# Kernel tuning notes

Hardware: AMD Instinct MI355X
Metric: run time of the kernel (lower is better)

Reference implementation:

```python
import jax, jax.numpy as jnp
import numpy as np

N, D, H = 2048, 128, 40


def setup_inputs() -> dict:
    key = jax.random.key(0)
    kx, kw, kv = jax.random.split(key, 3)
    X = jax.random.normal(kx, (N, D), dtype=jnp.float32)
    # nn.Parameter(torch.randn(D, D) / D) per head, stacked over H
    W = jax.random.normal(kw, (H, D, D), dtype=jnp.float32) / D
    V = jax.random.normal(kv, (H, D, D), dtype=jnp.float32) / D
    return {"X": X, "W": W, "V": V}


def reference(X, W, V):
    d = X.shape[1]
    # scores[h] = X @ W[h] @ X.T / sqrt(D)   -> [H, N, N]
    XW = jnp.einsum("nd,hde->hne", X, W)
    scores = jnp.einsum("hne,me->hnm", XW, X) / jnp.sqrt(jnp.asarray(d, X.dtype))
    # softmax over dim=1 of the 2D per-head score matrix == last axis here
    weights = jax.nn.softmax(scores, axis=-1) + 1e-8
    # A[h] = weights[h] @ X @ V[h]; output = sum over heads -> [N, D]
    XV = jnp.einsum("md,hde->hme", X, V)
    out = jnp.einsum("hnm,hme->ne", weights, XV)
    return out
```

## Files before the change

kernel.cpp:

```cpp
#include <hip/hip_runtime.h>
#include <hip/hip_bf16.h>
#include <stdint.h>

#define N 2048
#define D 128
#define H 40

typedef __attribute__((ext_vector_type(8))) short short8;
typedef __attribute__((ext_vector_type(4))) float float4v;
typedef __attribute__((ext_vector_type(8))) float float8v;
typedef __attribute__((ext_vector_type(16))) float float16v;
typedef __attribute__((ext_vector_type(8))) _Float16 half8v;

static __device__ __forceinline__ unsigned short f32_to_bf16(float f) {
  unsigned int u = __builtin_bit_cast(unsigned int, f);
  unsigned int rounding = 0x7FFFu + ((u >> 16) & 1u);
  return (unsigned short)((u + rounding) >> 16);
}

static __device__ __forceinline__ unsigned int pk2(float lo, float hi) {
  return (unsigned int)f32_to_bf16(lo) | ((unsigned int)f32_to_bf16(hi) << 16);
}

static __device__ __forceinline__ unsigned int pk2f(float lo, float hi) {
  unsigned int a = __builtin_bit_cast(unsigned int, lo) + 0x8000u;
  unsigned int b = __builtin_bit_cast(unsigned int, hi) + 0x8000u;
  return __builtin_amdgcn_perm(b, a, 0x07060302u);
}

static __device__ __forceinline__ unsigned long long pack4(float x0, float x1,
                                                           float x2, float x3) {
  return (unsigned long long)pk2(x0, x1) | ((unsigned long long)pk2(x2, x3) << 32);
}

static __device__ __forceinline__ float fast_exp2(float x) {
#if __has_builtin(__builtin_amdgcn_exp2f)
  return __builtin_amdgcn_exp2f(x);
#else
  return __expf(0.69314718056f * x);
#endif
}

static __device__ __forceinline__ void load_lds16(const void* g, void* l) {
  __builtin_amdgcn_global_load_lds(
      (const __attribute__((address_space(1))) unsigned int*)g,
      (__attribute__((address_space(3))) unsigned int*)l, 16, 0, 0);
}

#define MFMA32(a, b, c) __builtin_amdgcn_mfma_f32_32x32x16_bf16((a), (b), (c), 0, 0, 0)

static __device__ __forceinline__ void regs_to_bfrags(const float16v c, int hh,
                                                      short8& f0, short8& f1) {
  unsigned int a0 = pk2f(c[0], c[1]),   a1 = pk2f(c[2], c[3]);
  unsigned int a2 = pk2f(c[4], c[5]),   a3 = pk2f(c[6], c[7]);
  unsigned int a4 = pk2f(c[8], c[9]),   a5 = pk2f(c[10], c[11]);
  unsigned int a6 = pk2f(c[12], c[13]), a7 = pk2f(c[14], c[15]);
  unsigned int x0 = __shfl_xor(hh ? a0 : a2, 32);
  unsigned int x1 = __shfl_xor(hh ? a1 : a3, 32);
  unsigned int x2 = __shfl_xor(hh ? a4 : a6, 32);
  unsigned int x3 = __shfl_xor(hh ? a5 : a7, 32);
  uint4 u0 = {hh ? x0 : a0, hh ? x1 : a1, hh ? a2 : x0, hh ? a3 : x1};
  uint4 u1 = {hh ? x2 : a4, hh ? x3 : a5, hh ? a6 : x2, hh ? a7 : x3};
  f0 = __builtin_bit_cast(short8, u0);
  f1 = __builtin_bit_cast(short8, u1);
}

static __device__ __forceinline__ void regs_to_pfrags(const float16v s, int hh,
                                                      float& lsum, short8& f0,
                                                      short8& f1) {
  float e[16];
  float acc = 0.0f;
#pragma unroll
  for (int i = 0; i < 16; i++) { e[i] = fast_exp2(s[i]); acc += e[i]; }
  lsum += acc;
  unsigned int a0 = pk2f(e[0], e[1]),   a1 = pk2f(e[2], e[3]);
  unsigned int a2 = pk2f(e[4], e[5]),   a3 = pk2f(e[6], e[7]);
  unsigned int a4 = pk2f(e[8], e[9]),   a5 = pk2f(e[10], e[11]);
  unsigned int a6 = pk2f(e[12], e[13]), a7 = pk2f(e[14], e[15]);
  unsigned int x0 = __shfl_xor(hh ? a0 : a2, 32);
  unsigned int x1 = __shfl_xor(hh ? a1 : a3, 32);
  unsigned int x2 = __shfl_xor(hh ? a4 : a6, 32);
  unsigned int x3 = __shfl_xor(hh ? a5 : a7, 32);
  uint4 u0 = {hh ? x0 : a0, hh ? x1 : a1, hh ? a2 : x0, hh ? a3 : x1};
  uint4 u1 = {hh ? x2 : a4, hh ? x3 : a5, hh ? a6 : x2, hh ? a7 : x3};
  f0 = __builtin_bit_cast(short8, u0);
  f1 = __builtin_bit_cast(short8, u1);
}

static __device__ __forceinline__ void stage_64x256(const char* gbase, size_t stride,
                                                    int colOff, char* lds, int wave,
                                                    int lane) {
#pragma unroll
  for (int i = 0; i < 4; i++) {
    int r = wave * 16 + i * 4 + (lane >> 4);
    int us = (lane & 15) ^ (r & 15);
    load_lds16(gbase + (size_t)r * stride + colOff + us * 16,
               lds + (wave * 16 + i * 4) * 256);
  }
}
static __device__ __forceinline__ void stage_128x256(const char* gbase, size_t stride,
                                                     char* lds, int wave, int lane) {
#pragma unroll
  for (int i = 0; i < 8; i++) {
    int r = wave * 32 + i * 4 + (lane >> 4);
    int us = (lane & 15) ^ (r & 15);
    load_lds16(gbase + (size_t)r * stride + us * 16, lds + (wave * 32 + i * 4) * 256);
  }
}
static __device__ __forceinline__ void stage_128x128(const char* gbase, size_t stride,
                                                     int colOff, char* lds, int wave,
                                                     int lane) {
#pragma unroll
  for (int i = 0; i < 4; i++) {
    int m = wave * 16 + i * 4 + (lane >> 4);
    int u = (lane & 15) ^ (m & 15);
    int grow = 2 * m + (u >> 3);
    load_lds16(gbase + (size_t)grow * stride + colOff + (u & 7) * 16,
               lds + (wave * 16 + i * 4) * 256);
  }
}
static __device__ __forceinline__ short8 read_macro(const char* lds, int row, int kunit) {
  int m = row >> 1;
  int u = ((row & 1) << 3) | kunit;
  return *(const short8*)(lds + m * 256 + ((u ^ (m & 15)) * 16));
}

__global__ __launch_bounds__(256)
void xconv_kernel(const float* __restrict__ X, unsigned short* __restrict__ Xb,
                  unsigned short* __restrict__ XbT) {
  const int n0 = blockIdx.x * 128;
  const int tid = threadIdx.x;
  __shared__ __align__(16) unsigned short Lt[128 * 136];
  for (int i = tid; i < 128 * 32; i += 256) {
    int row = i >> 5, c4 = (i & 31) * 4;
    float4v x = *(const float4v*)(X + (size_t)(n0 + row) * D + c4);
    unsigned long long p = pack4(x.x, x.y, x.z, x.w);
    *(unsigned long long*)(Lt + row * 136 + c4) = p;
    *(unsigned long long*)(Xb + (size_t)(n0 + row) * D + c4) = p;
  }
  __syncthreads();
  for (int i = tid; i < 128 * 16; i += 256) {
    int d = i >> 4, g = i & 15;
    short8 v;
#pragma unroll
    for (int j = 0; j < 8; j++) v[j] = (short)Lt[(g * 8 + j) * 136 + d];
    *(short8*)(XbT + (size_t)d * N + n0 + g * 8) = v;
  }
}

__global__ __launch_bounds__(256)
void wvconv_kernel(const float* __restrict__ W, const float* __restrict__ V,
                   unsigned short* __restrict__ Wt, unsigned short* __restrict__ Vt) {
  const int b = blockIdx.x;
  const int mat = (b >= H) ? 1 : 0;
  const int h = mat ? b - H : b;
  const float* src = (mat ? V : W) + (size_t)h * D * D;
  unsigned short* dst = (mat ? Vt : Wt) + (size_t)h * D * D;
  const float scale = mat ? 1.0f : 0.1275174313f;
  const int tid = threadIdx.x;
  __shared__ __align__(16) unsigned short Lt[128 * 136];
  for (int i = tid; i < 128 * 32; i += 256) {
    int d = i >> 5, e4 = (i & 31) * 4;
    float4v w = *(const float4v*)(src + d * D + e4);
    Lt[(e4 + 0) * 136 + d] = f32_to_bf16(w.x * scale);
    Lt[(e4 + 1) * 136 + d] = f32_to_bf16(w.y * scale);
    Lt[(e4 + 2) * 136 + d] = f32_to_bf16(w.z * scale);
    Lt[(e4 + 3) * 136 + d] = f32_to_bf16(w.w * scale);
  }
  __syncthreads();
  for (int i = tid; i < 128 * 16; i += 256) {
    int e = i >> 4, u = i & 15;
    *(uint4*)((char*)dst + (size_t)e * 256 + u * 16) =
        *(const uint4*)((const char*)Lt + (size_t)e * 272 + u * 16);
  }
}

__global__ __launch_bounds__(256)
void attn_kernel(const unsigned short* __restrict__ Xb,
                 const unsigned short* __restrict__ XbT,
                 const unsigned short* __restrict__ Wt,
                 const unsigned short* __restrict__ Vt,
                 unsigned short* __restrict__ Opart, float* __restrict__ Lsum) {
  __shared__ __align__(16) char smem[32768];
  const int bx = blockIdx.x;
  const int kh = bx & 1;
  const int q0 = ((bx >> 1) & 15) << 7;
  const int h = bx >> 5;
  const int tid = threadIdx.x;
  const int wave = tid >> 6, lane = tid & 63;
  const int l = lane & 31, hh = lane >> 5;

  const char* XbB = (const char*)Xb;
  const char* XbTB = (const char*)XbT;
  const char* WtB = (const char*)(Wt + (size_t)h * D * D);
  const char* VtB = (const char*)(Vt + (size_t)h * D * D);

  float16v qa[4];
#pragma unroll
  for (int et = 0; et < 4; et++) qa[et] = (float16v)0.0f;
#pragma unroll
  for (int dh = 0; dh < 2; dh++) {
    __syncthreads();
    stage_128x128(XbB + (size_t)q0 * 256, 256, dh * 128, smem, wave, lane);
    stage_128x128(WtB, 256, dh * 128, smem + 16384, wave, lane);
    __syncthreads();
    short8 xfr[4];
#pragma unroll
    for (int dk = 0; dk < 4; dk++)
      xfr[dk] = read_macro(smem, wave * 32 + l, dk * 2 + hh);
#pragma unroll
    for (int et = 0; et < 4; et++)
#pragma unroll
      for (int dk = 0; dk < 4; dk++) {
        short8 wa = read_macro(smem + 16384, et * 32 + l, dk * 2 + hh);
        qa[et] = MFMA32(wa, xfr[dk], qa[et]);
      }
  }
  short8 qf[8];
#pragma unroll
  for (int et = 0; et < 4; et++)
    regs_to_bfrags(qa[et], hh, qf[2 * et], qf[2 * et + 1]);

  float16v Tacc[4];
#pragma unroll
  for (int dt = 0; dt < 4; dt++) Tacc[dt] = (float16v)0.0f;
  float lsum = 0.0f;

  const int kbase = kh * (N / 2);
  for (int kt = 0; kt < 16; kt++) {
    const int k0 = kbase + kt * 64;
    __syncthreads();
    stage_64x256(XbB + (size_t)k0 * 256, 256, 0, smem, wave, lane);
    stage_128x128(XbTB, 4096, k0 * 2, smem + 16384, wave, lane);
    __syncthreads();
#pragma unroll
    for (int ksub = 0; ksub < 2; ksub++) {
      float16v sa = (float16v)0.0f, sb = (float16v)0.0f;
      const int krow = ksub * 32 + l;
#pragma unroll
      for (int ks = 0; ks < 4; ks++) {
        short8 kfa = *(const short8*)(smem + krow * 256 +
                                      (((2 * ks + hh) ^ (krow & 15)) * 16));
        short8 kfb = *(const short8*)(smem + krow * 256 +
                                      (((2 * (ks + 4) + hh) ^ (krow & 15)) * 16));
        sa = MFMA32(kfa, qf[ks], sa);
        sb = MFMA32(kfb, qf[ks + 4], sb);
      }
      float16v s = sa + sb;
      short8 pf0, pf1;
      regs_to_pfrags(s, hh, lsum, pf0, pf1);
#pragma unroll
      for (int kk = 0; kk < 2; kk++) {
        short8 pf = kk ? pf1 : pf0;
#pragma unroll
        for (int dt = 0; dt < 4; dt++) {
          short8 xt = read_macro(smem + 16384, dt * 32 + l, ksub * 4 + kk * 2 + hh);
          Tacc[dt] = MFMA32(xt, pf, Tacc[dt]);
        }
      }
    }
  }

  float tot = lsum + __shfl_xor(lsum, 32);
  if (hh == 0) Lsum[(size_t)(h * 2 + kh) * N + q0 + wave * 32 + l] = tot;

  short8 tb[8];
#pragma unroll
  for (int dt = 0; dt < 4; dt++)
    regs_to_bfrags(Tacc[dt], hh, tb[2 * dt], tb[2 * dt + 1]);

  __syncthreads();
  stage_128x256(VtB, 256, smem, wave, lane);
  __syncthreads();

  float16v oacc[4];
#pragma unroll
  for (int et = 0; et < 4; et++) oacc[et] = (float16v)0.0f;
#pragma unroll
  for (int et = 0; et < 4; et++) {
    const int erow = et * 32 + l;
#pragma unroll
    for (int dk = 0; dk < 8; dk++) {
      short8 va = *(const short8*)(smem + erow * 256 +
                                   (((2 * dk + hh) ^ (erow & 15)) * 16));
      oacc[et] = MFMA32(va, tb[dk], oacc[et]);
    }
  }

  unsigned short* Oph = Opart + (size_t)(h * 2 + kh) * N * D;
#pragma unroll
  for (int pass = 0; pass < 2; pass++) {
    __syncthreads();
    const int qrow = wave * 32 + l;
#pragma unroll
    for (int etL = 0; etL < 2; etL++) {
      int et = pass * 2 + etL;
#pragma unroll
      for (int g = 0; g < 4; g++) {
        int unit = etL * 8 + 2 * g + hh;
        float4v v;
        v.x = oacc[et][4 * g + 0];
        v.y = oacc[et][4 * g + 1];
        v.z = oacc[et][4 * g + 2];
        v.w = oacc[et][4 * g + 3];
        *(float4v*)(smem + qrow * 256 + ((unit ^ (qrow & 15)) * 16)) = v;
      }
    }
    __syncthreads();
#pragma unroll
    for (int i = 0; i < 8; i++) {
      int idx = i * 256 + tid;
      int qr = idx >> 4, up = idx & 15, u = up ^ (qr & 15);
      float4v v = *(const float4v*)(smem + qr * 256 + up * 16);
      auto h0 = __builtin_amdgcn_cvt_pkrtz(v.x, v.y);
      auto h1 = __builtin_amdgcn_cvt_pkrtz(v.z, v.w);
      uint2 st = {__builtin_bit_cast(unsigned int, h0),
                  __builtin_bit_cast(unsigned int, h1)};
      *(uint2*)(Oph + (size_t)(q0 + qr) * D + pass * 64 + u * 4) = st;
    }
  }
}

__global__ __launch_bounds__(256)
void reduce_kernel(const unsigned short* __restrict__ Opart,
                   const float* __restrict__ Lsum, float* __restrict__ out) {
  int idx = blockIdx.x * 256 + threadIdx.x;
  int n = idx >> 4;
  const uint4* base = (const uint4*)Opart;
  float8v acc = (float8v)0.0f;
#pragma unroll 4
  for (int h = 0; h < H; h++) {
    float lt = Lsum[(size_t)(2 * h) * N + n] + Lsum[(size_t)(2 * h + 1) * N + n];
    float il = __builtin_amdgcn_rcpf(lt);
    uint4 a = base[(size_t)(2 * h) * (N * D / 8) + idx];
    uint4 b = base[(size_t)(2 * h + 1) * (N * D / 8) + idx];
    float8v fa = __builtin_convertvector(__builtin_bit_cast(half8v, a), float8v);
    float8v fb = __builtin_convertvector(__builtin_bit_cast(half8v, b), float8v);
    acc += (fa + fb) * il;
  }
  *(float8v*)(out + (size_t)idx * 8) = acc;
}

extern "C" void kernel_launch(void* const* d_in, const int* in_sizes, int n_in,
                              void* d_out, int out_size, void* d_ws, size_t ws_size,
                              hipStream_t stream) {
  const float* X = (const float*)d_in[0];
  const float* W = (const float*)d_in[1];
  const float* V = (const float*)d_in[2];
  float* out = (float*)d_out;

  unsigned short* Xb = (unsigned short*)d_ws;
  unsigned short* XbT = Xb + (size_t)N * D;
  unsigned short* Wt = XbT + (size_t)N * D;
  unsigned short* Vt = Wt + (size_t)H * D * D;
  unsigned short* Opart = Vt + (size_t)H * D * D;
  float* Lsum = (float*)(Opart + (size_t)H * 2 * N * D);

  xconv_kernel<<<dim3(N / 128), 256, 0, stream>>>(X, Xb, XbT);
  wvconv_kernel<<<dim3(2 * H), 256, 0, stream>>>(W, V, Wt, Vt);
  attn_kernel<<<dim3(16 * 2 * H), 256, 0, stream>>>(Xb, XbT, Wt, Vt, Opart, Lsum);
  reduce_kernel<<<dim3(N * D / 8 / 256), 256, 0, stream>>>(Opart, Lsum, out);
}
```

Baseline: 224.4 us.

## Double-buffer LDS staging to overlap global loads with MFMA compute

Shared memory grows to two 32KB buffers, so the next K/XT tile (and finally the V tile) is staged into one buffer while MFMAs run on the other. One barrier per iteration replaces two, and the Q-projection stages also prefetch ahead. Score accumulation is merged into a single MFMA chain instead of two partial accumulators. Doubling LDS use to 64KB may reduce occupancy, and the single accumulator lengthens the dependency chain.

```diff
diff --git a/kernel.cpp b/kernel.cpp
--- a/kernel.cpp
+++ b/kernel.cpp
@@ -5,6 +5,7 @@
 #define N 2048
 #define D 128
 #define H 40
+#define NT 16
 
 typedef __attribute__((ext_vector_type(8))) short short8;
 typedef __attribute__((ext_vector_type(4))) float float4v;
@@ -181,7 +182,9 @@
                  const unsigned short* __restrict__ Wt,
                  const unsigned short* __restrict__ Vt,
                  unsigned short* __restrict__ Opart, float* __restrict__ Lsum) {
-  __shared__ __align__(16) char smem[32768];
+  __shared__ __align__(16) char smem[65536];
+  char* buf0 = smem;
+  char* buf1 = smem + 32768;
   const int bx = blockIdx.x;
   const int kh = bx & 1;
   const int q0 = ((bx >> 1) & 15) << 7;
@@ -194,27 +197,43 @@
   const char* XbTB = (const char*)XbT;
   const char* WtB = (const char*)(Wt + (size_t)h * D * D);
   const char* VtB = (const char*)(Vt + (size_t)h * D * D);
+  const int kbase = kh * (N / 2);
+
+  stage_128x128(XbB + (size_t)q0 * 256, 256, 0, buf0, wave, lane);
+  stage_128x128(WtB, 256, 0, buf0 + 16384, wave, lane);
+  __syncthreads();
+  stage_128x128(XbB + (size_t)q0 * 256, 256, 128, buf1, wave, lane);
+  stage_128x128(WtB, 256, 128, buf1 + 16384, wave, lane);
 
   float16v qa[4];
 #pragma unroll
   for (int et = 0; et < 4; et++) qa[et] = (float16v)0.0f;
-#pragma unroll
-  for (int dh = 0; dh < 2; dh++) {
-    __syncthreads();
-    stage_128x128(XbB + (size_t)q0 * 256, 256, dh * 128, smem, wave, lane);
-    stage_128x128(WtB, 256, dh * 128, smem + 16384, wave, lane);
-    __syncthreads();
+  {
     short8 xfr[4];
 #pragma unroll
     for (int dk = 0; dk < 4; dk++)
-      xfr[dk] = read_macro(smem, wave * 32 + l, dk * 2 + hh);
+      xfr[dk] = read_macro(buf0, wave * 32 + l, dk * 2 + hh);
 #pragma unroll
     for (int et = 0; et < 4; et++)
 #pragma unroll
-      for (int dk = 0; dk < 4; dk++) {
-        short8 wa = read_macro(smem + 16384, et * 32 + l, dk * 2 + hh);
-        qa[et] = MFMA32(wa, xfr[dk], qa[et]);
-      }
+      for (int dk = 0; dk < 4; dk++)
+        qa[et] = MFMA32(read_macro(buf0 + 16384, et * 32 + l, dk * 2 + hh),
+                        xfr[dk], qa[et]);
+  }
+  __syncthreads();
+  stage_64x256(XbB + (size_t)kbase * 256, 256, 0, buf0, wave, lane);
+  stage_128x128(XbTB, 4096, kbase * 2, buf0 + 16384, wave, lane);
+  {
+    short8 xfr[4];
+#pragma unroll
+    for (int dk = 0; dk < 4; dk++)
+      xfr[dk] = read_macro(buf1, wave * 32 + l, dk * 2 + hh);
+#pragma unroll
+    for (int et = 0; et < 4; et++)
+#pragma unroll
+      for (int dk = 0; dk < 4; dk++)
+        qa[et] = MFMA32(read_macro(buf1 + 16384, et * 32 + l, dk * 2 + hh),
+                        xfr[dk], qa[et]);
   }
   short8 qf[8];
 #pragma unroll
@@ -225,28 +244,28 @@
 #pragma unroll
   for (int dt = 0; dt < 4; dt++) Tacc[dt] = (float16v)0.0f;
   float lsum = 0.0f;
-
-  const int kbase = kh * (N / 2);
-  for (int kt = 0; kt < 16; kt++) {
-    const int k0 = kbase + kt * 64;
-    __syncthreads();
-    stage_64x256(XbB + (size_t)k0 * 256, 256, 0, smem, wave, lane);
-    stage_128x128(XbTB, 4096, k0 * 2, smem + 16384, wave, lane);
-    __syncthreads();
+  __syncthreads();
+
+  for (int kt = 0; kt < NT; kt++) {
+    char* cur = (kt & 1) ? buf1 : buf0;
+    char* nxt = (kt & 1) ? buf0 : buf1;
+    if (kt + 1 < NT) {
+      const int k0n = kbase + (kt + 1) * 64;
+      stage_64x256(XbB + (size_t)k0n * 256, 256, 0, nxt, wave, lane);
+      stage_128x128(XbTB, 4096, k0n * 2, nxt + 16384, wave, lane);
+    } else {
+      stage_128x256(VtB, 256, nxt, wave, lane);
+    }
 #pragma unroll
     for (int ksub = 0; ksub < 2; ksub++) {
-      float16v sa = (float16v)0.0f, sb = (float16v)0.0f;
+      float16v s = (float16v)0.0f;
       const int krow = ksub * 32 + l;
 #pragma unroll
-      for (int ks = 0; ks < 4; ks++) {
-        short8 kfa = *(const short8*)(smem + krow * 256 +
-                                      (((2 * ks + hh) ^ (krow & 15)) * 16));
-        short8 kfb = *(const short8*)(smem + krow * 256 +
-                                      (((2 * (ks + 4) + hh) ^ (krow & 15)) * 16));
-        sa = MFMA32(kfa, qf[ks], sa);
-        sb = MFMA32(kfb, qf[ks + 4], sb);
+      for (int ks = 0; ks < 8; ks++) {
+        short8 kf = *(const short8*)(cur + krow * 256 +
+                                     (((2 * ks + hh) ^ (krow & 15)) * 16));
+        s = MFMA32(kf, qf[ks], s);
       }
-      float16v s = sa + sb;
       short8 pf0, pf1;
       regs_to_pfrags(s, hh, lsum, pf0, pf1);
 #pragma unroll
@@ -254,11 +273,12 @@
         short8 pf = kk ? pf1 : pf0;
 #pragma unroll
         for (int dt = 0; dt < 4; dt++) {
-          short8 xt = read_macro(smem + 16384, dt * 32 + l, ksub * 4 + kk * 2 + hh);
+          short8 xt = read_macro(cur + 16384, dt * 32 + l, ksub * 4 + kk * 2 + hh);
           Tacc[dt] = MFMA32(xt, pf, Tacc[dt]);
         }
       }
     }
+    __syncthreads();
   }
 
   float tot = lsum + __shfl_xor(lsum, 32);
@@ -269,10 +289,6 @@
   for (int dt = 0; dt < 4; dt++)
     regs_to_bfrags(Tacc[dt], hh, tb[2 * dt], tb[2 * dt + 1]);
 
-  __syncthreads();
-  stage_128x256(VtB, 256, smem, wave, lane);
-  __syncthreads();
-
   float16v oacc[4];
 #pragma unroll
   for (int et = 0; et < 4; et++) oacc[et] = (float16v)0.0f;
@@ -281,7 +297,7 @@
     const int erow = et * 32 + l;
 #pragma unroll
     for (int dk = 0; dk < 8; dk++) {
-      short8 va = *(const short8*)(smem + erow * 256 +
+      short8 va = *(const short8*)(buf0 + erow * 256 +
                                    (((2 * dk + hh) ^ (erow & 15)) * 16));
       oacc[et] = MFMA32(va, tb[dk], oacc[et]);
     }
@@ -303,7 +319,7 @@
         v.y = oacc[et][4 * g + 1];
         v.z = oacc[et][4 * g + 2];
         v.w = oacc[et][4 * g + 3];
-        *(float4v*)(smem + qrow * 256 + ((unit ^ (qrow & 15)) * 16)) = v;
+        *(float4v*)(buf1 + qrow * 256 + ((unit ^ (qrow & 15)) * 16)) = v;
       }
     }
     __syncthreads();
@@ -311,7 +327,7 @@
     for (int i = 0; i < 8; i++) {
       int idx = i * 256 + tid;
       int qr = idx >> 4, up = idx & 15, u = up ^ (qr & 15);
-      float4v v = *(const float4v*)(smem + qr * 256 + up * 16);
+      float4v v = *(const float4v*)(buf1 + qr * 256 + up * 16);
       auto h0 = __builtin_amdgcn_cvt_pkrtz(v.x, v.y);
       auto h1 = __builtin_amdgcn_cvt_pkrtz(v.z, v.w);
       uint2 st = {__builtin_bit_cast(unsigned int, h0),
```

Result: faster. 201.7 us (-10.1%).
